# Kernel tuning notes

Measured on AMD Instinct MI355X. Metric: run time of the kernel, lower is better.

## Reference

```python
import jax, jax.numpy as jnp
import numpy as np

MAX_LEN = 2048
D_MODEL = 1024
NUM_HEADS = 16
D_HEAD = D_MODEL // NUM_HEADS
BATCH = 2
SEQ = 2048


def setup_inputs() -> dict:
    key = jax.random.key(0)
    ks = jax.random.split(key, 8)
    scale = 1.0 / np.sqrt(D_MODEL)
    return {
        "x": jax.random.normal(ks[0], (BATCH, SEQ, D_MODEL), dtype=jnp.float32),
        "Wq": jax.random.normal(ks[1], (D_MODEL, D_MODEL), dtype=jnp.float32) * scale,
        "bq": jnp.zeros((D_MODEL,), dtype=jnp.float32),
        "Wk": jax.random.normal(ks[2], (D_MODEL, D_MODEL), dtype=jnp.float32) * scale,
        "bk": jnp.zeros((D_MODEL,), dtype=jnp.float32),
        "Wv": jax.random.normal(ks[3], (D_MODEL, D_MODEL), dtype=jnp.float32) * scale,
        "bv": jnp.zeros((D_MODEL,), dtype=jnp.float32),
        "Er": jax.random.normal(ks[4], (MAX_LEN, D_HEAD), dtype=jnp.float32),
    }


def _skew(QEr):
    # QEr: [B, H, S, S] -> Transformer-XL skew -> Srel: [B, H, S, S]
    B, H, S, _ = QEr.shape
    padded = jnp.pad(QEr, ((0, 0), (0, 0), (0, 0), (1, 0)))  # [B,H,S,S+1]
    reshaped = padded.reshape(B, H, S + 1, S)
    return reshaped[:, :, 1:, :]


def reference(x, Wq, bq, Wk, bk, Wv, bv, Er):
    B, S, D = x.shape
    H, dh = NUM_HEADS, D // NUM_HEADS
    q = (x @ Wq + bq).reshape(B, S, H, dh).transpose(0, 2, 1, 3)  # [B,H,S,dh]
    k = (x @ Wk + bk).reshape(B, S, H, dh).transpose(0, 2, 1, 3)
    v = (x @ Wv + bv).reshape(B, S, H, dh).transpose(0, 2, 1, 3)
    Er_s = Er[MAX_LEN - S:, :]                                    # [S, dh]
    QEr = jnp.einsum("bhsd,ld->bhsl", q, Er_s)                    # [B,H,S,S]
    Srel = _skew(QEr)
    QKt = jnp.einsum("bhsd,bhtd->bhst", q, k)
    attn = (QKt + Srel) / jnp.sqrt(jnp.asarray(dh, x.dtype))
    causal = jnp.tril(jnp.ones((S, S), dtype=bool))
    attn = jnp.where(causal[None, None], attn, -jnp.inf)
    attn = jax.nn.softmax(attn, axis=-1)
    out = jnp.einsum("bhst,bhtd->bhsd", attn, v)                  # [B,H,S,dh]
    return out.transpose(0, 2, 1, 3).reshape(B, S, D)             # dropout in eval = identity
```

## Files before the change

### kernel.cpp

```cpp
#include <hip/hip_runtime.h>
#include <hip/hip_bf16.h>

#define SLEN   2048
#define DMODEL 1024
#define NHEADS 16
#define DHEAD  64
#define NBATCH 2
#define EPAD_ROWS 2432

#define QSCALE 0.18033688011112042f
#define EXPB   23.083120654223414f

typedef __bf16 bf16x8 __attribute__((ext_vector_type(8)));
typedef float  f32x4  __attribute__((ext_vector_type(4)));

__device__ __forceinline__ unsigned short f2bf(float f) {
    unsigned int u = __builtin_bit_cast(unsigned int, f);
    return (unsigned short)((u + 0x7fffu + ((u >> 16) & 1u)) >> 16);
}

__device__ __forceinline__ float exp2_hw(float x) {
    float r;
    asm("v_exp_f32 %0, %1" : "=v"(r) : "v"(x));
    return r;
}

__device__ __forceinline__ unsigned int cvtpk_bf16(float lo, float hi) {
    unsigned int d;
    asm("v_cvt_pk_bf16_f32 %0, %1, %2" : "=v"(d) : "v"(lo), "v"(hi));
    return d;
}

__device__ __forceinline__ bf16x8 ld8(const unsigned short* p) {
    union { uint4 u; bf16x8 b; } t;
    t.u = *(const uint4*)p;
    return t.b;
}

__device__ __forceinline__ void glds16(const unsigned short* g, unsigned short* l) {
    __builtin_amdgcn_global_load_lds(
        (const __attribute__((address_space(1))) unsigned int*)g,
        (__attribute__((address_space(3))) unsigned int*)l, 16, 0, 0);
}

__global__ __launch_bounds__(256) void prep_kernel(
    const float* __restrict__ x, const float* __restrict__ Er,
    const float* __restrict__ Wq, const float* __restrict__ Wk,
    const float* __restrict__ Wv,
    unsigned short* __restrict__ xb, unsigned short* __restrict__ Ep,
    unsigned short* __restrict__ Wt) {
    const int bi = blockIdx.x, tid = threadIdx.x;
    if (bi < 4096) {
        int i = (bi * 256 + tid) * 4;
        float4 v = *(const float4*)(x + i);
        ushort4 o;
        o.x = f2bf(v.x); o.y = f2bf(v.y); o.z = f2bf(v.z); o.w = f2bf(v.w);
        *(ushort4*)(xb + i) = o;
    } else if (bi < 4704) {
        int i = (bi - 4096) * 256 + tid;
        int row = i >> 6;
        unsigned short v = 0;
        if (row < SLEN) v = f2bf(Er[i]);
        Ep[i] = v;
    } else {
        __shared__ float tile[32][33];
        const int b3 = bi - 4704;
        const int z = b3 >> 10, rem = b3 & 1023;
        const int n0 = (rem & 31) * 32, k0 = (rem >> 5) * 32;
        const float* W = (z == 0) ? Wq : (z == 1 ? Wk : Wv);
        unsigned short* out = Wt + (size_t)z * DMODEL * DMODEL;
        const int tx = tid & 31, ty = tid >> 5;
        for (int r = 0; r < 32; r += 8)
            tile[ty + r][tx] = W[(size_t)(k0 + ty + r) * DMODEL + n0 + tx];
        __syncthreads();
        for (int r = 0; r < 32; r += 8)
            out[(size_t)(n0 + ty + r) * DMODEL + k0 + tx] = f2bf(tile[tx][ty + r]);
    }
}

__global__ __launch_bounds__(256, 2) void qkv_gemm(
    const unsigned short* __restrict__ xb, const unsigned short* __restrict__ Wt,
    const float* __restrict__ bq, const float* __restrict__ bk, const float* __restrict__ bv,
    unsigned short* __restrict__ Qs, unsigned short* __restrict__ Ks,
    unsigned short* __restrict__ Vts) {
    const int b = blockIdx.x;
    const int mt = b & 31, nt = b >> 5;
    const int m0 = mt * 128, n0 = nt * 64;

    __shared__ __align__(16) unsigned short As[128][64];
    __shared__ __align__(16) unsigned short Bs[3][64][64];

    const int tid = threadIdx.x;
    const int wave = tid >> 6, lane = tid & 63, l16 = lane & 15, quad = lane >> 4;
    const int wm = (wave >> 1) * 64, wn2 = (wave & 1) * 32;

    const int lr8 = lane >> 3;
    const int sc  = ((lane & 7) ^ lr8) * 8;

    f32x4 accQ[4][2], accK[4][2], accV[2][4];
#pragma unroll
    for (int mi = 0; mi < 4; mi++)
#pragma unroll
        for (int ni = 0; ni < 2; ni++) {
            accQ[mi][ni] = (f32x4){0.f, 0.f, 0.f, 0.f};
            accK[mi][ni] = (f32x4){0.f, 0.f, 0.f, 0.f};
            accV[ni][mi] = (f32x4){0.f, 0.f, 0.f, 0.f};
        }

    for (int j = 0; j < 16; ++j) {
        if (j) __syncthreads();
        const int k0 = j * 64;
#pragma unroll
        for (int c = 0; c < 4; c++) {
            const int seg = wave * 4 + c;
            glds16(&xb[(size_t)(m0 + seg * 8 + lr8) * DMODEL + k0 + sc], &As[seg * 8][0]);
        }
#pragma unroll
        for (int c = 0; c < 6; c++) {
            const int idx = wave * 6 + c;
            const int z = idx >> 3, seg = idx & 7;
            glds16(&Wt[(size_t)z * DMODEL * DMODEL + (size_t)(n0 + seg * 8 + lr8) * DMODEL + k0 + sc],
                   &Bs[z][seg * 8][0]);
        }
        __syncthreads();

#pragma unroll
        for (int ks = 0; ks < 2; ks++) {
            const int pc = ((ks * 4 + quad) ^ (l16 & 7)) * 8;
            bf16x8 a[4], bb[3][2];
#pragma unroll
            for (int mi = 0; mi < 4; mi++) a[mi] = ld8(&As[wm + mi * 16 + l16][pc]);
#pragma unroll
            for (int z = 0; z < 3; z++)
#pragma unroll
                for (int ni = 0; ni < 2; ni++) bb[z][ni] = ld8(&Bs[z][wn2 + ni * 16 + l16][pc]);
#pragma unroll
            for (int mi = 0; mi < 4; mi++)
#pragma unroll
                for (int ni = 0; ni < 2; ni++) {
                    accQ[mi][ni] = __builtin_amdgcn_mfma_f32_16x16x32_bf16(a[mi], bb[0][ni], accQ[mi][ni], 0, 0, 0);
                    accK[mi][ni] = __builtin_amdgcn_mfma_f32_16x16x32_bf16(a[mi], bb[1][ni], accK[mi][ni], 0, 0, 0);
                    accV[ni][mi] = __builtin_amdgcn_mfma_f32_16x16x32_bf16(bb[2][ni], a[mi], accV[ni][mi], 0, 0, 0);
                }
        }
    }

    const int hh = n0 >> 6;

#pragma unroll
    for (int ni = 0; ni < 2; ni++) {
        const int n = n0 + wn2 + ni * 16 + l16;
        const float bqv = bq[n], bkv = bk[n];
        const int d = n & 63;
#pragma unroll
        for (int mi = 0; mi < 4; mi++)
#pragma unroll
            for (int r = 0; r < 4; r++) {
                const int m = m0 + wm + mi * 16 + quad * 4 + r;
                const int bi = m >> 11, s = m & 2047;
                Qs[((size_t)(bi * NHEADS + hh) * SLEN + s) * 64 + d] =
                    f2bf((accQ[mi][ni][r] + bqv) * QSCALE);
                Ks[((size_t)(bi * NHEADS + hh) * SLEN + s) * 64 + d] =
                    f2bf(accK[mi][ni][r] + bkv);
            }
    }
#pragma unroll
    for (int ni = 0; ni < 2; ni++)
#pragma unroll
        for (int r = 0; r < 4; r++) {
            const int n = n0 + wn2 + ni * 16 + quad * 4 + r;
            const float bvv = bv[n];
            const int d = n & 63;
#pragma unroll
            for (int mi = 0; mi < 4; mi++) {
                const int m = m0 + wm + mi * 16 + l16;
                const int bi = m >> 11, s = m & 2047;
                Vts[((size_t)((bi * NHEADS + hh) * 64 + d)) * SLEN + s] =
                    f2bf(accV[ni][mi][r] + bvv);
            }
        }
}

__global__ __launch_bounds__(256, 2) void attn_kernel(
    const unsigned short* __restrict__ Q,
    const unsigned short* __restrict__ K,
    const unsigned short* __restrict__ Vt,
    const unsigned short* __restrict__ Ep,
    float* __restrict__ out) {
    const int tid = threadIdx.x;
    const int wave = tid >> 6, lane = tid & 63, l16 = lane & 15, quad = lane >> 4;
    const int lr8 = lane >> 3;
    const int swz = ((lane & 7) ^ lr8) * 8;

    const int bh = blockIdx.x & 31;
    const int pg = blockIdx.x >> 5;

    __shared__ __align__(16) unsigned short Ksh[2][64 * 64];
    __shared__ __align__(16) unsigned short Vsh[2][64 * 64];
    __shared__ __align__(16) unsigned short Esh[256 * 64];

    const unsigned short* Qb = Q + (size_t)bh * SLEN * 64;
    const unsigned short* Kb = K + (size_t)bh * SLEN * 64;
    const unsigned short* Vb = Vt + (size_t)bh * 64 * SLEN;
    const int ob = bh >> 4, oh = bh & 15;

    const int pc0 = (quad ^ (l16 & 7)) * 8;
    const int pc1 = ((4 + quad) ^ (l16 & 7)) * 8;
    const int krot = (15 - l16) & 3;
    const bool c1 = (krot & 1) != 0, c2 = (krot & 2) != 0;
    int permE[4]; bool hiE[4];
#pragma unroll
    for (int r = 0; r < 4; r++) {
        const int idx = quad * 4 + r + 15 - l16;
        permE[r] = ((idx >> 2) & 3) * 16 + l16;
        const int c  = r + 15 - l16;
        const int qv = (quad - (c >> 2)) & 3;
        hiE[r] = (qv * 4 + c) >= 16;
    }

    int s0 = pg * 64;
    int ntp = pg + 1;

#pragma unroll 1
    for (int pass = 0; pass < 2; ++pass) {
        const int sw = s0 + 16 * wave;
        const bf16x8 aq0 = ld8(Qb + (size_t)(sw + l16) * 64 + quad * 8);
        const bf16x8 aq1 = ld8(Qb + (size_t)(sw + l16) * 64 + 32 + quad * 8);

        f32x4 accO[4];
        float sacc[4];
#pragma unroll
        for (int nt = 0; nt < 4; nt++) accO[nt] = (f32x4){0.f, 0.f, 0.f, 0.f};
#pragma unroll
        for (int r = 0; r < 4; r++) sacc[r] = 0.f;

        const int p0row = SLEN - 64 - s0;

#pragma unroll
        for (int c = 0; c < 2; c++) {
            const int seg = wave * 2 + c;
            glds16(&Kb[(size_t)(seg * 8 + lr8) * 64 + swz], &Ksh[0][seg * 8 * 64]);
            glds16(&Vb[(size_t)(seg * 8 + lr8) * SLEN + swz], &Vsh[0][seg * 8 * 64]);
        }
#pragma unroll
        for (int u = 0; u < 6; u++) {
            const int idx = wave * 6 + u;
            const int grow = p0row + idx * 8;
            glds16(&Ep[(size_t)(grow + lr8) * 64 + swz], &Esh[(grow & 255) * 64]);
        }
        __syncthreads();

        f32x4 carryE = (f32x4){0.f, 0.f, 0.f, 0.f};

        for (int j = 0; j < ntp; ++j) {
            const int t0 = j * 64;
            const int cur = j & 1;

            if (j + 1 < ntp) {
                const int t1 = t0 + 64, nb = cur ^ 1;
#pragma unroll
                for (int c = 0; c < 2; c++) {
                    const int seg = wave * 2 + c;
                    glds16(&Kb[(size_t)(t1 + seg * 8 + lr8) * 64 + swz], &Ksh[nb][seg * 8 * 64]);
                    glds16(&Vb[(size_t)(seg * 8 + lr8) * SLEN + t1 + swz], &Vsh[nb][seg * 8 * 64]);
                }
                const int er = p0row + t0 + 128;
#pragma unroll
                for (int c = 0; c < 2; c++) {
                    const int seg = wave * 2 + c;
                    glds16(&Ep[(size_t)(er + seg * 8 + lr8) * 64 + swz],
                           &Esh[((er + seg * 8) & 255) * 64]);
                }
            }

            f32x4 accS[4];
#pragma unroll
            for (int nt = 0; nt < 4; nt++)
                accS[nt] = (f32x4){-EXPB, -EXPB, -EXPB, -EXPB};
#pragma unroll
            for (int nt = 0; nt < 4; nt++) {
                bf16x8 bk0 = ld8(&Ksh[cur][(nt * 16 + l16) * 64 + pc0]);
                bf16x8 bk1 = ld8(&Ksh[cur][(nt * 16 + l16) * 64 + pc1]);
                accS[nt] = __builtin_amdgcn_mfma_f32_16x16x32_bf16(bk0, aq0, accS[nt], 0, 0, 0);
                accS[nt] = __builtin_amdgcn_mfma_f32_16x16x32_bf16(bk1, aq1, accS[nt], 0, 0, 0);
            }

            const int rm0 = (SLEN - 16 - sw + t0) & 255;
            f32x4 accE[5];
            if (j == 0) {
                accE[0] = (f32x4){0.f, 0.f, 0.f, 0.f};
                const int rowm = (rm0 + l16) & 255;
                bf16x8 be0 = ld8(&Esh[rowm * 64 + pc0]);
                bf16x8 be1 = ld8(&Esh[rowm * 64 + pc1]);
                accE[0] = __builtin_amdgcn_mfma_f32_16x16x32_bf16(be0, aq0, accE[0], 0, 0, 0);
                accE[0] = __builtin_amdgcn_mfma_f32_16x16x32_bf16(be1, aq1, accE[0], 0, 0, 0);
            } else {
                accE[0] = carryE;
            }
#pragma unroll
            for (int nt = 1; nt < 5; nt++) {
                accE[nt] = (f32x4){0.f, 0.f, 0.f, 0.f};
                const int rowm = (rm0 + nt * 16 + l16) & 255;
                bf16x8 be0 = ld8(&Esh[rowm * 64 + pc0]);
                bf16x8 be1 = ld8(&Esh[rowm * 64 + pc1]);
                accE[nt] = __builtin_amdgcn_mfma_f32_16x16x32_bf16(be0, aq0, accE[nt], 0, 0, 0);
                accE[nt] = __builtin_amdgcn_mfma_f32_16x16x32_bf16(be1, aq1, accE[nt], 0, 0, 0);
            }
            carryE = accE[4];

            f32x4 rotE[5];
#pragma unroll
            for (int g = 0; g < 5; g++) {
                f32x4 A = accE[g], t, rt;
#pragma unroll
                for (int r = 0; r < 4; r++) t[r] = c1 ? A[(r + 1) & 3] : A[r];
#pragma unroll
                for (int r = 0; r < 4; r++) rt[r] = c2 ? t[(r + 2) & 3] : t[r];
                rotE[g] = rt;
            }

            float pe[4][4];
            auto scoreblk = [&](bool masked) {
#pragma unroll
                for (int nt = 0; nt < 4; nt++) {
#pragma unroll
                    for (int r = 0; r < 4; r++) {
                        float send = hiE[r] ? rotE[nt + 1][r] : rotE[nt][r];
                        float rel = __shfl(send, permE[r]);
                        float p = exp2_hw(accS[nt][r] + rel);
                        if (masked)
                            p = (t0 + nt * 16 + quad * 4 + r <= sw + l16) ? p : 0.0f;
                        sacc[r] += p;
                        pe[nt][r] = p;
                    }
                }
            };
            if (t0 + 63 <= sw) scoreblk(false);
            else               scoreblk(true);

            unsigned int w[4][2];
#pragma unroll
            for (int nt = 0; nt < 4; nt++) {
                w[nt][0] = cvtpk_bf16(pe[nt][0], pe[nt][1]);
                w[nt][1] = cvtpk_bf16(pe[nt][2], pe[nt][3]);
            }
            bf16x8 pf[2];
#pragma unroll
            for (int c = 0; c < 2; c++) {
                unsigned int a0 = w[2 * c][0], b0 = w[2 * c + 1][0];
                unsigned int a1 = w[2 * c][1], b1 = w[2 * c + 1][1];
                asm volatile("v_permlane32_swap_b32 %0, %1" : "+v"(a0), "+v"(b0));
                asm volatile("v_permlane16_swap_b32 %0, %1" : "+v"(a0), "+v"(b0));
                asm volatile("v_permlane32_swap_b32 %0, %1" : "+v"(a1), "+v"(b1));
                asm volatile("v_permlane16_swap_b32 %0, %1" : "+v"(a1), "+v"(b1));
                union { uint4 u; bf16x8 b; } t;
                t.u = (uint4){a0, a1, b0, b1};
                pf[c] = t.b;
            }

#pragma unroll
            for (int ntd = 0; ntd < 4; ntd++) {
                bf16x8 bv0 = ld8(&Vsh[cur][(ntd * 16 + l16) * 64 + pc0]);
                bf16x8 bv1 = ld8(&Vsh[cur][(ntd * 16 + l16) * 64 + pc1]);
                accO[ntd] = __builtin_amdgcn_mfma_f32_16x16x32_bf16(bv0, pf[0], accO[ntd], 0, 0, 0);
                accO[ntd] = __builtin_amdgcn_mfma_f32_16x16x32_bf16(bv1, pf[1], accO[ntd], 0, 0, 0);
            }

            __syncthreads();
        }

        float s4 = (sacc[0] + sacc[1]) + (sacc[2] + sacc[3]);
        s4 += __shfl_xor(s4, 16);
        s4 += __shfl_xor(s4, 32);
        const float inv = 1.f / s4;
        const int srow = sw + l16;
        float* orow = out + ((size_t)(ob * SLEN + srow)) * DMODEL + oh * 64 + quad * 4;
#pragma unroll
        for (int ntd = 0; ntd < 4; ntd++) {
            float4 st = {accO[ntd][0] * inv, accO[ntd][1] * inv,
                         accO[ntd][2] * inv, accO[ntd][3] * inv};
            *(float4*)(orow + ntd * 16) = st;
        }

        s0 = (31 - pg) * 64;
        ntp = 32 - pg;
    }
}

extern "C" void kernel_launch(void* const* d_in, const int* in_sizes, int n_in,
                              void* d_out, int out_size, void* d_ws, size_t ws_size,
                              hipStream_t stream) {
    const float* x  = (const float*)d_in[0];
    const float* Wq = (const float*)d_in[1];
    const float* bq = (const float*)d_in[2];
    const float* Wk = (const float*)d_in[3];
    const float* bk = (const float*)d_in[4];
    const float* Wv = (const float*)d_in[5];
    const float* bv = (const float*)d_in[6];
    const float* Er = (const float*)d_in[7];
    float* out = (float*)d_out;

    char* p = (char*)d_ws;
    unsigned short* xb  = (unsigned short*)p; p += (size_t)4096 * 1024 * 2;
    unsigned short* Wt  = (unsigned short*)p; p += (size_t)3 * 1024 * 1024 * 2;
    unsigned short* Qs  = (unsigned short*)p; p += (size_t)32 * 2048 * 64 * 2;
    unsigned short* Ks  = (unsigned short*)p; p += (size_t)32 * 2048 * 64 * 2;
    unsigned short* Vts = (unsigned short*)p; p += (size_t)32 * 2048 * 64 * 2;
    unsigned short* Ep  = (unsigned short*)p; p += (size_t)EPAD_ROWS * 64 * 2;

    hipLaunchKernelGGL(prep_kernel, dim3(7776), dim3(256), 0, stream,
                       x, Er, Wq, Wk, Wv, xb, Ep, Wt);
    hipLaunchKernelGGL(qkv_gemm, dim3(512), dim3(256), 0, stream,
                       xb, Wt, bq, bk, bv, Qs, Ks, Vts);
    hipLaunchKernelGGL(attn_kernel, dim3(512), dim3(256), 0, stream, Qs, Ks, Vts, Ep, out);
}
```

Measured before the change: 171.1 us.

## Split paired query tiles into separate blocks and shrink LDS for higher occupancy

Each attention block previously handled two mirrored query tiles (pg and 31-pg) in two passes to balance causal work. Now each block handles one query tile, launches 1024 blocks ordered longest-first, single-buffers K (with an extra barrier after the QK MFMAs before prefetching), and shrinks the E ring buffer from 256 to 192 rows. Occupancy is raised to 3 blocks per SIMD group via launch bounds. This trades explicit load pairing and some K-prefetch overlap for more resident waves and dynamic scheduling, and may add register pressure.

Measured after the change: 168.8 us. Within noise of the previous version (-1.3%).

```diff
diff --git a/kernel.cpp b/kernel.cpp
--- a/kernel.cpp
+++ b/kernel.cpp
@@ -181,7 +181,7 @@
         }
 }
 
-__global__ __launch_bounds__(256, 2) void attn_kernel(
+__global__ __launch_bounds__(256, 3) void attn_kernel(
     const unsigned short* __restrict__ Q,
     const unsigned short* __restrict__ K,
     const unsigned short* __restrict__ Vt,
@@ -193,11 +193,13 @@
     const int swz = ((lane & 7) ^ lr8) * 8;
 
     const int bh = blockIdx.x & 31;
-    const int pg = blockIdx.x >> 5;
-
-    __shared__ __align__(16) unsigned short Ksh[2][64 * 64];
+    const int qt = 31 - (blockIdx.x >> 5);
+    const int s0 = qt * 64;
+    const int ntp = qt + 1;
+
+    __shared__ __align__(16) unsigned short Ksh[64 * 64];
     __shared__ __align__(16) unsigned short Vsh[2][64 * 64];
-    __shared__ __align__(16) unsigned short Esh[256 * 64];
+    __shared__ __align__(16) unsigned short Esh[192 * 64];
 
     const unsigned short* Qb = Q + (size_t)bh * SLEN * 64;
     const unsigned short* Kb = K + (size_t)bh * SLEN * 64;
@@ -218,172 +220,168 @@
         hiE[r] = (qv * 4 + c) >= 16;
     }
 
-    int s0 = pg * 64;
-    int ntp = pg + 1;
-
-#pragma unroll 1
-    for (int pass = 0; pass < 2; ++pass) {
-        const int sw = s0 + 16 * wave;
-        const bf16x8 aq0 = ld8(Qb + (size_t)(sw + l16) * 64 + quad * 8);
-        const bf16x8 aq1 = ld8(Qb + (size_t)(sw + l16) * 64 + 32 + quad * 8);
-
-        f32x4 accO[4];
-        float sacc[4];
-#pragma unroll
-        for (int nt = 0; nt < 4; nt++) accO[nt] = (f32x4){0.f, 0.f, 0.f, 0.f};
-#pragma unroll
-        for (int r = 0; r < 4; r++) sacc[r] = 0.f;
-
-        const int p0row = SLEN - 64 - s0;
-
-#pragma unroll
-        for (int c = 0; c < 2; c++) {
-            const int seg = wave * 2 + c;
-            glds16(&Kb[(size_t)(seg * 8 + lr8) * 64 + swz], &Ksh[0][seg * 8 * 64]);
-            glds16(&Vb[(size_t)(seg * 8 + lr8) * SLEN + swz], &Vsh[0][seg * 8 * 64]);
-        }
-#pragma unroll
-        for (int u = 0; u < 6; u++) {
-            const int idx = wave * 6 + u;
-            const int grow = p0row + idx * 8;
-            glds16(&Ep[(size_t)(grow + lr8) * 64 + swz], &Esh[(grow & 255) * 64]);
-        }
+    const int sw = s0 + 16 * wave;
+    const bf16x8 aq0 = ld8(Qb + (size_t)(sw + l16) * 64 + quad * 8);
+    const bf16x8 aq1 = ld8(Qb + (size_t)(sw + l16) * 64 + 32 + quad * 8);
+
+    f32x4 accO[4];
+    float sacc[4];
+#pragma unroll
+    for (int nt = 0; nt < 4; nt++) accO[nt] = (f32x4){0.f, 0.f, 0.f, 0.f};
+#pragma unroll
+    for (int r = 0; r < 4; r++) sacc[r] = 0.f;
+
+    const int p0row = SLEN - 64 - s0;
+
+#pragma unroll
+    for (int c = 0; c < 2; c++) {
+        const int seg = wave * 2 + c;
+        glds16(&Kb[(size_t)(seg * 8 + lr8) * 64 + swz], &Ksh[seg * 8 * 64]);
+        glds16(&Vb[(size_t)(seg * 8 + lr8) * SLEN + swz], &Vsh[0][seg * 8 * 64]);
+    }
+#pragma unroll
+    for (int u = 0; u < 4; u++) {
+        const int idx = wave * 4 + u;
+        glds16(&Ep[(size_t)(p0row + idx * 8 + lr8) * 64 + swz], &Esh[idx * 8 * 64]);
+    }
+    __syncthreads();
+
+    f32x4 carryE = (f32x4){0.f, 0.f, 0.f, 0.f};
+    int rb = 48 - 16 * wave;
+    int ed = 128;
+
+    for (int j = 0; j < ntp; ++j) {
+        const int t0 = j * 64;
+        const int cur = j & 1;
+
+        f32x4 accS[4];
+#pragma unroll
+        for (int nt = 0; nt < 4; nt++)
+            accS[nt] = (f32x4){-EXPB, -EXPB, -EXPB, -EXPB};
+#pragma unroll
+        for (int nt = 0; nt < 4; nt++) {
+            bf16x8 bk0 = ld8(&Ksh[(nt * 16 + l16) * 64 + pc0]);
+            bf16x8 bk1 = ld8(&Ksh[(nt * 16 + l16) * 64 + pc1]);
+            accS[nt] = __builtin_amdgcn_mfma_f32_16x16x32_bf16(bk0, aq0, accS[nt], 0, 0, 0);
+            accS[nt] = __builtin_amdgcn_mfma_f32_16x16x32_bf16(bk1, aq1, accS[nt], 0, 0, 0);
+        }
+
         __syncthreads();
 
-        f32x4 carryE = (f32x4){0.f, 0.f, 0.f, 0.f};
-
-        for (int j = 0; j < ntp; ++j) {
-            const int t0 = j * 64;
-            const int cur = j & 1;
-
-            if (j + 1 < ntp) {
-                const int t1 = t0 + 64, nb = cur ^ 1;
-#pragma unroll
-                for (int c = 0; c < 2; c++) {
-                    const int seg = wave * 2 + c;
-                    glds16(&Kb[(size_t)(t1 + seg * 8 + lr8) * 64 + swz], &Ksh[nb][seg * 8 * 64]);
-                    glds16(&Vb[(size_t)(seg * 8 + lr8) * SLEN + t1 + swz], &Vsh[nb][seg * 8 * 64]);
-                }
-                const int er = p0row + t0 + 128;
-#pragma unroll
-                for (int c = 0; c < 2; c++) {
-                    const int seg = wave * 2 + c;
-                    glds16(&Ep[(size_t)(er + seg * 8 + lr8) * 64 + swz],
-                           &Esh[((er + seg * 8) & 255) * 64]);
+        if (j + 1 < ntp) {
+            const int t1 = t0 + 64, nb = cur ^ 1;
+#pragma unroll
+            for (int c = 0; c < 2; c++) {
+                const int seg = wave * 2 + c;
+                glds16(&Kb[(size_t)(t1 + seg * 8 + lr8) * 64 + swz], &Ksh[seg * 8 * 64]);
+                glds16(&Vb[(size_t)(seg * 8 + lr8) * SLEN + t1 + swz], &Vsh[nb][seg * 8 * 64]);
+            }
+            const int er = p0row + t0 + 128;
+#pragma unroll
+            for (int c = 0; c < 2; c++) {
+                const int seg = wave * 2 + c;
+                glds16(&Ep[(size_t)(er + seg * 8 + lr8) * 64 + swz],
+                       &Esh[(ed + seg * 8) * 64]);
+            }
+        }
+
+        const int base = rb + l16;
+        f32x4 accE[5];
+        if (j == 0) {
+            accE[0] = (f32x4){0.f, 0.f, 0.f, 0.f};
+            bf16x8 be0 = ld8(&Esh[base * 64 + pc0]);
+            bf16x8 be1 = ld8(&Esh[base * 64 + pc1]);
+            accE[0] = __builtin_amdgcn_mfma_f32_16x16x32_bf16(be0, aq0, accE[0], 0, 0, 0);
+            accE[0] = __builtin_amdgcn_mfma_f32_16x16x32_bf16(be1, aq1, accE[0], 0, 0, 0);
+        } else {
+            accE[0] = carryE;
+        }
+#pragma unroll
+        for (int nt = 1; nt < 5; nt++) {
+            int row = base + nt * 16;
+            if (row >= 192) row -= 192;
+            accE[nt] = (f32x4){0.f, 0.f, 0.f, 0.f};
+            bf16x8 be0 = ld8(&Esh[row * 64 + pc0]);
+            bf16x8 be1 = ld8(&Esh[row * 64 + pc1]);
+            accE[nt] = __builtin_amdgcn_mfma_f32_16x16x32_bf16(be0, aq0, accE[nt], 0, 0, 0);
+            accE[nt] = __builtin_amdgcn_mfma_f32_16x16x32_bf16(be1, aq1, accE[nt], 0, 0, 0);
+        }
+        carryE = accE[4];
+        rb += 64; if (rb >= 192) rb -= 192;
+        ed += 64; if (ed >= 192) ed -= 192;
+
+        f32x4 rotE[5];
+#pragma unroll
+        for (int g = 0; g < 5; g++) {
+            f32x4 A = accE[g], t, rt;
+#pragma unroll
+            for (int r = 0; r < 4; r++) t[r] = c1 ? A[(r + 1) & 3] : A[r];
+#pragma unroll
+            for (int r = 0; r < 4; r++) rt[r] = c2 ? t[(r + 2) & 3] : t[r];
+            rotE[g] = rt;
+        }
+
+        float pe[4][4];
+        auto scoreblk = [&](bool masked) {
+#pragma unroll
+            for (int nt = 0; nt < 4; nt++) {
+#pragma unroll
+                for (int r = 0; r < 4; r++) {
+                    float send = hiE[r] ? rotE[nt + 1][r] : rotE[nt][r];
+                    float rel = __shfl(send, permE[r]);
+                    float p = exp2_hw(accS[nt][r] + rel);
+                    if (masked)
+                        p = (t0 + nt * 16 + quad * 4 + r <= sw + l16) ? p : 0.0f;
+                    sacc[r] += p;
+                    pe[nt][r] = p;
                 }
             }
-
-            f32x4 accS[4];
-#pragma unroll
-            for (int nt = 0; nt < 4; nt++)
-                accS[nt] = (f32x4){-EXPB, -EXPB, -EXPB, -EXPB};
-#pragma unroll
-            for (int nt = 0; nt < 4; nt++) {
-                bf16x8 bk0 = ld8(&Ksh[cur][(nt * 16 + l16) * 64 + pc0]);
-                bf16x8 bk1 = ld8(&Ksh[cur][(nt * 16 + l16) * 64 + pc1]);
-                accS[nt] = __builtin_amdgcn_mfma_f32_16x16x32_bf16(bk0, aq0, accS[nt], 0, 0, 0);
-                accS[nt] = __builtin_amdgcn_mfma_f32_16x16x32_bf16(bk1, aq1, accS[nt], 0, 0, 0);
-            }
-
-            const int rm0 = (SLEN - 16 - sw + t0) & 255;
-            f32x4 accE[5];
-            if (j == 0) {
-                accE[0] = (f32x4){0.f, 0.f, 0.f, 0.f};
-                const int rowm = (rm0 + l16) & 255;
-                bf16x8 be0 = ld8(&Esh[rowm * 64 + pc0]);
-                bf16x8 be1 = ld8(&Esh[rowm * 64 + pc1]);
-                accE[0] = __builtin_amdgcn_mfma_f32_16x16x32_bf16(be0, aq0, accE[0], 0, 0, 0);
-                accE[0] = __builtin_amdgcn_mfma_f32_16x16x32_bf16(be1, aq1, accE[0], 0, 0, 0);
-            } else {
-                accE[0] = carryE;
-            }
-#pragma unroll
-            for (int nt = 1; nt < 5; nt++) {
-                accE[nt] = (f32x4){0.f, 0.f, 0.f, 0.f};
-                const int rowm = (rm0 + nt * 16 + l16) & 255;
-                bf16x8 be0 = ld8(&Esh[rowm * 64 + pc0]);
-                bf16x8 be1 = ld8(&Esh[rowm * 64 + pc1]);
-                accE[nt] = __builtin_amdgcn_mfma_f32_16x16x32_bf16(be0, aq0, accE[nt], 0, 0, 0);
-                accE[nt] = __builtin_amdgcn_mfma_f32_16x16x32_bf16(be1, aq1, accE[nt], 0, 0, 0);
-            }
-            carryE = accE[4];
-
-            f32x4 rotE[5];
-#pragma unroll
-            for (int g = 0; g < 5; g++) {
-                f32x4 A = accE[g], t, rt;
-#pragma unroll
-                for (int r = 0; r < 4; r++) t[r] = c1 ? A[(r + 1) & 3] : A[r];
-#pragma unroll
-                for (int r = 0; r < 4; r++) rt[r] = c2 ? t[(r + 2) & 3] : t[r];
-                rotE[g] = rt;
-            }
-
-            float pe[4][4];
-            auto scoreblk = [&](bool masked) {
-#pragma unroll
-                for (int nt = 0; nt < 4; nt++) {
-#pragma unroll
-                    for (int r = 0; r < 4; r++) {
-                        float send = hiE[r] ? rotE[nt + 1][r] : rotE[nt][r];
-                        float rel = __shfl(send, permE[r]);
-                        float p = exp2_hw(accS[nt][r] + rel);
-                        if (masked)
-                            p = (t0 + nt * 16 + quad * 4 + r <= sw + l16) ? p : 0.0f;
-                        sacc[r] += p;
-                        pe[nt][r] = p;
-                    }
-                }
-            };
-            if (t0 + 63 <= sw) scoreblk(false);
-            else               scoreblk(true);
-
-            unsigned int w[4][2];
-#pragma unroll
-            for (int nt = 0; nt < 4; nt++) {
-                w[nt][0] = cvtpk_bf16(pe[nt][0], pe[nt][1]);
-                w[nt][1] = cvtpk_bf16(pe[nt][2], pe[nt][3]);
-            }
-            bf16x8 pf[2];
-#pragma unroll
-            for (int c = 0; c < 2; c++) {
-                unsigned int a0 = w[2 * c][0], b0 = w[2 * c + 1][0];
-                unsigned int a1 = w[2 * c][1], b1 = w[2 * c + 1][1];
-                asm volatile("v_permlane32_swap_b32 %0, %1" : "+v"(a0), "+v"(b0));
-                asm volatile("v_permlane16_swap_b32 %0, %1" : "+v"(a0), "+v"(b0));
-                asm volatile("v_permlane32_swap_b32 %0, %1" : "+v"(a1), "+v"(b1));
-                asm volatile("v_permlane16_swap_b32 %0, %1" : "+v"(a1), "+v"(b1));
-                union { uint4 u; bf16x8 b; } t;
-                t.u = (uint4){a0, a1, b0, b1};
-                pf[c] = t.b;
-            }
-
-#pragma unroll
-            for (int ntd = 0; ntd < 4; ntd++) {
-                bf16x8 bv0 = ld8(&Vsh[cur][(ntd * 16 + l16) * 64 + pc0]);
-                bf16x8 bv1 = ld8(&Vsh[cur][(ntd * 16 + l16) * 64 + pc1]);
-                accO[ntd] = __builtin_amdgcn_mfma_f32_16x16x32_bf16(bv0, pf[0], accO[ntd], 0, 0, 0);
-                accO[ntd] = __builtin_amdgcn_mfma_f32_16x16x32_bf16(bv1, pf[1], accO[ntd], 0, 0, 0);
-            }
-
-            __syncthreads();
-        }
-
-        float s4 = (sacc[0] + sacc[1]) + (sacc[2] + sacc[3]);
-        s4 += __shfl_xor(s4, 16);
-        s4 += __shfl_xor(s4, 32);
-        const float inv = 1.f / s4;
-        const int srow = sw + l16;
-        float* orow = out + ((size_t)(ob * SLEN + srow)) * DMODEL + oh * 64 + quad * 4;
+        };
+        if (t0 + 63 <= sw) scoreblk(false);
+        else               scoreblk(true);
+
+        unsigned int w[4][2];
+#pragma unroll
+        for (int nt = 0; nt < 4; nt++) {
+            w[nt][0] = cvtpk_bf16(pe[nt][0], pe[nt][1]);
+            w[nt][1] = cvtpk_bf16(pe[nt][2], pe[nt][3]);
+        }
+        bf16x8 pf[2];
+#pragma unroll
+        for (int c = 0; c < 2; c++) {
+            unsigned int a0 = w[2 * c][0], b0 = w[2 * c + 1][0];
+            unsigned int a1 = w[2 * c][1], b1 = w[2 * c + 1][1];
+            asm volatile("v_permlane32_swap_b32 %0, %1" : "+v"(a0), "+v"(b0));
+            asm volatile("v_permlane16_swap_b32 %0, %1" : "+v"(a0), "+v"(b0));
+            asm volatile("v_permlane32_swap_b32 %0, %1" : "+v"(a1), "+v"(b1));
+            asm volatile("v_permlane16_swap_b32 %0, %1" : "+v"(a1), "+v"(b1));
+            union { uint4 u; bf16x8 b; } t;
+            t.u = (uint4){a0, a1, b0, b1};
+            pf[c] = t.b;
+        }
+
 #pragma unroll
         for (int ntd = 0; ntd < 4; ntd++) {
-            float4 st = {accO[ntd][0] * inv, accO[ntd][1] * inv,
-                         accO[ntd][2] * inv, accO[ntd][3] * inv};
-            *(float4*)(orow + ntd * 16) = st;
-        }
-
-        s0 = (31 - pg) * 64;
-        ntp = 32 - pg;
+            bf16x8 bv0 = ld8(&Vsh[cur][(ntd * 16 + l16) * 64 + pc0]);
+            bf16x8 bv1 = ld8(&Vsh[cur][(ntd * 16 + l16) * 64 + pc1]);
+            accO[ntd] = __builtin_amdgcn_mfma_f32_16x16x32_bf16(bv0, pf[0], accO[ntd], 0, 0, 0);
+            accO[ntd] = __builtin_amdgcn_mfma_f32_16x16x32_bf16(bv1, pf[1], accO[ntd], 0, 0, 0);
+        }
+
+        __syncthreads();
+    }
+
+    float s4 = (sacc[0] + sacc[1]) + (sacc[2] + sacc[3]);
+    s4 += __shfl_xor(s4, 16);
+    s4 += __shfl_xor(s4, 32);
+    const float inv = 1.f / s4;
+    const int srow = sw + l16;
+    float* orow = out + ((size_t)(ob * SLEN + srow)) * DMODEL + oh * 64 + quad * 4;
+#pragma unroll
+    for (int ntd = 0; ntd < 4; ntd++) {
+        float4 st = {accO[ntd][0] * inv, accO[ntd][1] * inv,
+                     accO[ntd][2] * inv, accO[ntd][3] * inv};
+        *(float4*)(orow + ntd * 16) = st;
     }
 }
 
@@ -412,5 +410,5 @@
                        x, Er, Wq, Wk, Wv, xb, Ep, Wt);
     hipLaunchKernelGGL(qkv_gemm, dim3(512), dim3(256), 0, stream,
                        xb, Wt, bq, bk, bv, Qs, Ks, Vts);
-    hipLaunchKernelGGL(attn_kernel, dim3(512), dim3(256), 0, stream, Qs, Ks, Vts, Ep, out);
-}
+    hipLaunchKernelGGL(attn_kernel, dim3(1024), dim3(256), 0, stream, Qs, Ks, Vts, Ep, out);
+}
```
